# Kernel tuning notes

Hardware: AMD Instinct MI355X
Metric: run time of the kernel (lower is better)

The kernel has to match this reference:

```python
import jax, jax.numpy as jnp
import numpy as np

B, S, D, H, DFF, L, V = 2, 1024, 1280, 16, 8192, 4, 32000
DH = D // H
EPS = 1e-6


def positional_encoding(position, d_model):
    pos = np.arange(position)[:, None].astype(np.float32)
    i = np.arange(d_model)[None, :].astype(np.float32)
    angle = pos / np.power(10000.0, (2.0 * (i // 2)) / np.float32(d_model))
    sines = np.sin(angle[:, 0::2])
    cosines = np.cos(angle[:, 1::2])
    return jnp.asarray(np.concatenate([sines, cosines], axis=-1), dtype=jnp.float32)


def layer_norm(x, g, b):
    mu = jnp.mean(x, axis=-1, keepdims=True)
    var = jnp.mean(jnp.square(x - mu), axis=-1, keepdims=True)
    return (x - mu) * jax.lax.rsqrt(var + EPS) * g + b


def setup_inputs() -> dict:
    key = jax.random.key(0)
    ks = jax.random.split(key, 8)
    sc = 0.02
    return {
        "input_ids": jax.random.randint(ks[0], (B, S), 0, V, dtype=jnp.int64),
        "emb": jax.random.normal(ks[1], (V, D), jnp.float32) * sc,
        "Wq": jax.random.normal(ks[2], (L, D, D), jnp.float32) * sc,
        "Wk": jax.random.normal(ks[3], (L, D, D), jnp.float32) * sc,
        "Wv": jax.random.normal(ks[4], (L, D, D), jnp.float32) * sc,
        "Wo": jax.random.normal(ks[5], (L, D, D), jnp.float32) * sc,
        "bq": jnp.zeros((L, D)), "bk": jnp.zeros((L, D)),
        "bv": jnp.zeros((L, D)), "bo": jnp.zeros((L, D)),
        "W1": jax.random.normal(ks[6], (L, D, DFF), jnp.float32) * sc,
        "b1": jnp.zeros((L, DFF)),
        "W2": jax.random.normal(ks[7], (L, DFF, D), jnp.float32) * sc,
        "b2": jnp.zeros((L, D)),
        "ln1_g": jnp.ones((L, D)), "ln1_b": jnp.zeros((L, D)),
        "ln2_g": jnp.ones((L, D)), "ln2_b": jnp.zeros((L, D)),
        "lnf_g": jnp.ones((D,)), "lnf_b": jnp.zeros((D,)),
    }


def _forward(input_ids, emb, Wq, bq, Wk, bk, Wv, bv, Wo, bo,
             W1, b1, W2, b2, ln1_g, ln1_b, ln2_g, ln2_b, lnf_g, lnf_b):
    # embedding scaled by sqrt(d_model) + fixed sinusoidal positions
    x = emb[input_ids] * jnp.sqrt(jnp.float32(D)) + positional_encoding(S, D)[None]
    # CTRL causal mask: 1 above the diagonal, contributes mask * -1e4 to logits
    neg_mask = jnp.triu(jnp.ones((S, S), jnp.float32), k=1) * -10000.0
    inv_sqrt_dk = 1.0 / jnp.sqrt(jnp.float32(DH))

    def block(x, p):
        (wq, bq_, wk, bk_, wv, bv_, wo, bo_,
         w1, b1_, w2, b2_, g1, be1, g2, be2) = p
        n = layer_norm(x, g1, be1)
        q = (n @ wq + bq_).reshape(B, S, H, DH).transpose(0, 2, 1, 3)  # [B,H,S,DH]
        k = (n @ wk + bk_).reshape(B, S, H, DH).transpose(0, 2, 1, 3)
        v = (n @ wv + bv_).reshape(B, S, H, DH).transpose(0, 2, 1, 3)
        logits = jnp.einsum("bhqd,bhkd->bhqk", q, k) * inv_sqrt_dk + neg_mask
        attn = jax.nn.softmax(logits, axis=-1)
        ctx = jnp.einsum("bhqk,bhkd->bhqd", attn, v)
        ctx = ctx.transpose(0, 2, 1, 3).reshape(B, S, D)
        x = x + ctx @ wo + bo_
        n2 = layer_norm(x, g2, be2)
        x = x + jax.nn.relu(n2 @ w1 + b1_) @ w2 + b2_
        return x, None

    params = (Wq, bq, Wk, bk, Wv, bv, Wo, bo, W1, b1, W2, b2,
              ln1_g, ln1_b, ln2_g, ln2_b)
    x, _ = jax.lax.scan(block, x, params)
    return layer_norm(x, lnf_g, lnf_b)


def reference(input_ids, emb, Wq, Wk, Wv, Wo, bq, bk, bv, bo,
              W1, b1, W2, b2, ln1_g, ln1_b, ln2_g, ln2_b, lnf_g, lnf_b):
    return _forward(input_ids, emb, Wq, bq, Wk, bk, Wv, bv, Wo, bo,
                    W1, b1, W2, b2, ln1_g, ln1_b, ln2_g, ln2_b, lnf_g, lnf_b)
```

## Files before the change

### kernel.cpp

```cpp
#include <hip/hip_runtime.h>


typedef unsigned short ushort_t;
typedef __attribute__((ext_vector_type(8))) __bf16 bf16x8;
typedef __attribute__((ext_vector_type(4))) float f32x4;

typedef const __attribute__((address_space(1))) unsigned int gu32;
typedef __attribute__((address_space(3))) unsigned int lu32;

#define DEV __device__ __forceinline__

DEV float bf2f(ushort_t h) { return __uint_as_float(((unsigned)h) << 16); }
DEV ushort_t f2bf(float f) {
    unsigned u = __float_as_uint(f);
    unsigned r = (u + 0x7fffu + ((u >> 16) & 1u)) >> 16;
    return (ushort_t)r;
}

DEV void async16(const void* g, void* l) {
    __builtin_amdgcn_global_load_lds((gu32*)g, (lu32*)l, 16, 0, 0);
}

__global__ __launch_bounds__(256) void embed_k(const int* __restrict__ ids,
                                               const float* __restrict__ emb,
                                               float* __restrict__ x) {
    __shared__ int flag64;
    const int r = blockIdx.x, t = threadIdx.x;
    if (t == 0) {
        int z = 0;
        for (int i = 1; i < 256; i += 2) z |= ids[i];
        flag64 = (z == 0);
    }
    __syncthreads();
    const long id = flag64 ? (long)((const long long*)ids)[r] : (long)ids[r];
    const float* er = emb + (size_t)id * 1280;
    const float pos = (float)(r & 1023);
    #pragma unroll
    for (int i = 0; i < 5; i++) {
        const int c = t + i * 256;
        float pe;
        if (c < 640) {
            float w = expf(-(float)c * 0.0143911568312128f);
            pe = sinf(pos * w);
        } else {
            float w = expf(-(float)(c - 640) * 0.0143911568312128f);
            pe = cosf(pos * w);
        }
        x[(size_t)r * 1280 + c] = er[c] * 35.77708763999664f + pe;
    }
}

template <typename OUT>
__global__ __launch_bounds__(256) void layernorm_k(const float* __restrict__ x,
                                                   const float* __restrict__ gw,
                                                   const float* __restrict__ bw,
                                                   OUT* __restrict__ out) {
    __shared__ float red[8];
    const int row = blockIdx.x, t = threadIdx.x;
    const float* xr = x + (size_t)row * 1280;
    float v[5], s = 0.f, ss = 0.f;
    #pragma unroll
    for (int i = 0; i < 5; i++) {
        v[i] = xr[t + i * 256];
        s += v[i];
        ss += v[i] * v[i];
    }
    #pragma unroll
    for (int o = 32; o; o >>= 1) {
        s += __shfl_xor(s, o, 64);
        ss += __shfl_xor(ss, o, 64);
    }
    if ((t & 63) == 0) { red[t >> 6] = s; red[4 + (t >> 6)] = ss; }
    __syncthreads();
    s = red[0] + red[1] + red[2] + red[3];
    ss = red[4] + red[5] + red[6] + red[7];
    const float mean = s * (1.f / 1280.f);
    const float var = ss * (1.f / 1280.f) - mean * mean;
    const float rs = rsqrtf(var + 1e-6f);
    #pragma unroll
    for (int i = 0; i < 5; i++) {
        const int c = t + i * 256;
        const float o = (v[i] - mean) * rs * gw[c] + bw[c];
        if constexpr (sizeof(OUT) == 2) out[(size_t)row * 1280 + c] = f2bf(o);
        else                            out[(size_t)row * 1280 + c] = o;
    }
}

__global__ __launch_bounds__(256) void convtrans_k(const float* __restrict__ src,
                                                   ushort_t* __restrict__ dst,
                                                   int R, int C) {
    __shared__ float tile[64][65];
    const int bx = blockIdx.x * 64;
    const int by = blockIdx.y * 64;
    const int c = threadIdx.x & 63;
    const int r0 = threadIdx.x >> 6;
    #pragma unroll
    for (int r = r0; r < 64; r += 4)
        tile[r][c] = src[(size_t)(by + r) * C + bx + c];
    __syncthreads();
    #pragma unroll
    for (int j = r0; j < 64; j += 4)
        dst[(size_t)(bx + j) * R + by + c] = f2bf(tile[c][j]);
}

__global__ __launch_bounds__(256) void softmax_k(const float* __restrict__ S,
                                                 ushort_t* __restrict__ P) {
    __shared__ float red[4];
    const size_t row = blockIdx.x;
    const int t = threadIdx.x;
    const float* sr = S + row * 1024;
    float v[4], m = -1e30f;
    #pragma unroll
    for (int i = 0; i < 4; i++) {
        v[i] = sr[t + i * 256];
        m = fmaxf(m, v[i]);
    }
    #pragma unroll
    for (int o = 32; o; o >>= 1) m = fmaxf(m, __shfl_xor(m, o, 64));
    if ((t & 63) == 0) red[t >> 6] = m;
    __syncthreads();
    m = fmaxf(fmaxf(red[0], red[1]), fmaxf(red[2], red[3]));
    float s = 0.f;
    #pragma unroll
    for (int i = 0; i < 4; i++) {
        v[i] = __expf(v[i] - m);
        s += v[i];
    }
    #pragma unroll
    for (int o = 32; o; o >>= 1) s += __shfl_xor(s, o, 64);
    __syncthreads();
    if ((t & 63) == 0) red[t >> 6] = s;
    __syncthreads();
    s = red[0] + red[1] + red[2] + red[3];
    const float inv = 1.f / s;
    #pragma unroll
    for (int i = 0; i < 4; i++)
        P[row * 1024 + t + i * 256] = f2bf(v[i] * inv);
}

__global__ void zero_k(float4* __restrict__ p) {
    p[(size_t)blockIdx.x * 256 + threadIdx.x] = make_float4(0.f, 0.f, 0.f, 0.f);
}

enum { EPI_QKV = 0, EPI_RELU = 1, EPI_RESID = 2, EPI_SC = 3, EPI_CTX = 4 };

template <int EPI>
__global__ __launch_bounds__(256, 2) void gemm_bt(
    const ushort_t* __restrict__ A, const ushort_t* __restrict__ Bt,
    const float* __restrict__ bias, const float* __restrict__ bias2,
    const float* __restrict__ bias3, float* __restrict__ outF,
    ushort_t* __restrict__ outB, ushort_t* __restrict__ outB2,
    ushort_t* __restrict__ outB3,
    int K, int lda, int ldb, int nAlloc, int ldc,
    long aStr, long bStr, long cStr, int g0, float scaleP) {
    __shared__ __align__(16) ushort_t As[128 * 32];
    __shared__ __align__(16) ushort_t Bs[128 * 32];

    const int t = threadIdx.x;
    const int lane = t & 63, wave = t >> 6;
    const int wm = wave >> 1, wn = wave & 1;
    const int l16 = lane & 15, quad = lane >> 4;
    const int tileM = blockIdx.y * 128, tileN = blockIdx.x * 128;
    const long z = blockIdx.z;

    const ushort_t* Ab = A + z * aStr;
    const ushort_t* Bb = Bt + z * bStr;

    int kBeg = 0, kEnd = K;
    if (EPI == EPI_RESID) {
        const int kc = K / (int)gridDim.z;
        kBeg = (int)z * kc;
        kEnd = kBeg + kc;
    }

    const int rowS = t >> 2;
    const int kb = (t & 3) * 16;

    const int rb0 = min(tileN + rowS, nAlloc - 1);
    const int rb1 = min(tileN + rowS + 64, nAlloc - 1);

    const char* apc0 = (const char*)Ab + ((size_t)(tileM + rowS) * lda + kBeg) * 2 + kb;
    const char* apc1 = apc0 + (size_t)64 * lda * 2;
    const char* bpc0 = (const char*)Bb + ((size_t)rb0 * ldb + kBeg) * 2 + kb;
    const char* bpc1 = (const char*)Bb + ((size_t)rb1 * ldb + kBeg) * 2 + kb;

    char* lA0 = (char*)As + wave * 1024;
    char* lA1 = lA0 + 4096;
    char* lB0 = (char*)Bs + wave * 1024;
    char* lB1 = lB0 + 4096;

    f32x4 acc[4][4] = {};

    for (int k0 = kBeg; k0 < kEnd; k0 += 32) {
        async16(apc0, lA0);
        async16(apc1, lA1);
        async16(bpc0, lB0);
        async16(bpc1, lB1);
        apc0 += 64; apc1 += 64; bpc0 += 64; bpc1 += 64;
        __syncthreads();

        bf16x8 af[4], bfv[4];
        #pragma unroll
        for (int i = 0; i < 4; i++)
            af[i] = *(const bf16x8*)&As[(wm * 64 + i * 16 + l16) * 32 + quad * 8];
        #pragma unroll
        for (int j = 0; j < 4; j++)
            bfv[j] = *(const bf16x8*)&Bs[(wn * 64 + j * 16 + l16) * 32 + quad * 8];
        #pragma unroll
        for (int i = 0; i < 4; i++)
            #pragma unroll
            for (int j = 0; j < 4; j++)
                acc[i][j] = __builtin_amdgcn_mfma_f32_16x16x32_bf16(af[i], bfv[j], acc[i][j], 0, 0, 0);
        __syncthreads();
    }

    #pragma unroll
    for (int i = 0; i < 4; i++) {
        const int r0 = tileM + wm * 64 + i * 16 + quad * 4;
        #pragma unroll
        for (int j = 0; j < 4; j++) {
            const int c = tileN + wn * 64 + j * 16 + l16;
            float bv = 0.f;
            if (EPI == EPI_QKV) {
                const float* bp = bias;
                int cc = c;
                if (c >= 2560) { cc = c - 2560; bp = bias3; }
                else if (c >= 1280) { cc = c - 1280; bp = bias2; }
                bv = bp[cc];
            } else if (EPI == EPI_RELU) {
                bv = bias[c];
            } else if (EPI == EPI_RESID) {
                bv = (z == 0) ? bias[c] : 0.f;
            }
            #pragma unroll
            for (int g = 0; g < 4; g++) {
                const int r = r0 + g;
                const float v = acc[i][j][g] + bv;
                if (EPI == EPI_QKV) {
                    int cc = c;
                    ushort_t* ob = outB;
                    bool isV = false;
                    if (c >= 2560) { cc = c - 2560; ob = outB3; isV = true; }
                    else if (c >= 1280) { cc = c - 1280; ob = outB2; }
                    const int b = r >> 10, s = r & 1023;
                    const int h = cc / 80, d = cc - h * 80;
                    if (isV) ob[((size_t)((b * 16 + h) * 96 + d)) * 1024 + s] = f2bf(v);
                    else     ob[((size_t)((b * 16 + h) * 1024 + s)) * 96 + d] = f2bf(v);
                } else if (EPI == EPI_RELU) {
                    outB[(size_t)r * ldc + c] = f2bf(fmaxf(v, 0.f));
                } else if (EPI == EPI_RESID) {
                    atomicAdd(outF + (size_t)r * ldc + c, v);
                } else if (EPI == EPI_SC) {
                    float sv = acc[i][j][g] * scaleP;
                    if (c > r) sv -= 10000.f;
                    outF[z * cStr + (size_t)r * ldc + c] = sv;
                } else {
                    if (c < 80) {
                        const int gg = g0 + (int)z;
                        const int b = gg >> 4, h = gg & 15;
                        outB[((size_t)(b * 1024 + r)) * 1280 + h * 80 + c] = f2bf(acc[i][j][g]);
                    }
                }
            }
        }
    }
}

extern "C" void kernel_launch(void* const* d_in, const int* in_sizes, int n_in,
                              void* d_out, int out_size, void* d_ws, size_t ws_size,
                              hipStream_t stream) {
    const int* ids = (const int*)d_in[0];
    const float* emb = (const float*)d_in[1];
    const float* Wq = (const float*)d_in[2];
    const float* Wk = (const float*)d_in[3];
    const float* Wv = (const float*)d_in[4];
    const float* Wo = (const float*)d_in[5];
    const float* bq = (const float*)d_in[6];
    const float* bk = (const float*)d_in[7];
    const float* bv = (const float*)d_in[8];
    const float* bo = (const float*)d_in[9];
    const float* W1 = (const float*)d_in[10];
    const float* b1 = (const float*)d_in[11];
    const float* W2 = (const float*)d_in[12];
    const float* b2 = (const float*)d_in[13];
    const float* ln1g = (const float*)d_in[14];
    const float* ln1b = (const float*)d_in[15];
    const float* ln2g = (const float*)d_in[16];
    const float* ln2b = (const float*)d_in[17];
    const float* lnfg = (const float*)d_in[18];
    const float* lnfb = (const float*)d_in[19];
    (void)in_sizes; (void)n_in; (void)out_size; (void)ws_size;

    char* p = (char*)d_ws;
    float* xf = (float*)p;          p += (size_t)2048 * 1280 * 4;
    ushort_t* nbuf = (ushort_t*)p;  p += (size_t)2048 * 1280 * 2;
    ushort_t* qp = (ushort_t*)p;    p += (size_t)32 * 1024 * 96 * 2;
    ushort_t* kp = (ushort_t*)p;    p += (size_t)32 * 1024 * 96 * 2;
    ushort_t* vT = (ushort_t*)p;    p += (size_t)32 * 96 * 1024 * 2;
    ushort_t* ctx = (ushort_t*)p;   p += (size_t)2048 * 1280 * 2;
    ushort_t* h1 = (ushort_t*)p;    p += (size_t)2048 * 8192 * 2;
    ushort_t* WT = (ushort_t*)p;    p += (size_t)8192 * 1280 * 2;
    float* Sb = (float*)h1;
    ushort_t* Pb = WT;
    const int CH = 8;

    const float scaleP = 0.11180339887498948f;

    embed_k<<<2048, 256, 0, stream>>>(ids, emb, xf);
    zero_k<<<4608, 256, 0, stream>>>((float4*)qp);

    for (int l = 0; l < 4; l++) {
        const float* Wq_l = Wq + (size_t)l * 1638400;
        const float* Wk_l = Wk + (size_t)l * 1638400;
        const float* Wv_l = Wv + (size_t)l * 1638400;
        const float* Wo_l = Wo + (size_t)l * 1638400;
        const float* W1_l = W1 + (size_t)l * 10485760;
        const float* W2_l = W2 + (size_t)l * 10485760;

        layernorm_k<ushort_t><<<2048, 256, 0, stream>>>(xf, ln1g + l * 1280, ln1b + l * 1280, nbuf);

        convtrans_k<<<dim3(20, 20), 256, 0, stream>>>(Wq_l, WT, 1280, 1280);
        convtrans_k<<<dim3(20, 20), 256, 0, stream>>>(Wk_l, WT + (size_t)1280 * 1280, 1280, 1280);
        convtrans_k<<<dim3(20, 20), 256, 0, stream>>>(Wv_l, WT + (size_t)2560 * 1280, 1280, 1280);
        gemm_bt<EPI_QKV><<<dim3(30, 16, 1), 256, 0, stream>>>(
            nbuf, WT, bq + l * 1280, bk + l * 1280, bv + l * 1280,
            nullptr, qp, kp, vT, 1280, 1280, 1280, 3840, 0, 0, 0, 0, 0, 0.f);

        for (int c0 = 0; c0 < 32; c0 += CH) {
            gemm_bt<EPI_SC><<<dim3(8, 8, CH), 256, 0, stream>>>(
                qp + (size_t)c0 * 98304, kp + (size_t)c0 * 98304, nullptr, nullptr, nullptr,
                Sb, nullptr, nullptr, nullptr,
                96, 96, 96, 1024, 1024, 98304, 98304, 1048576, 0, scaleP);
            softmax_k<<<CH * 1024, 256, 0, stream>>>(Sb, Pb);
            gemm_bt<EPI_CTX><<<dim3(1, 8, CH), 256, 0, stream>>>(
                Pb, vT + (size_t)c0 * 98304, nullptr, nullptr, nullptr,
                nullptr, ctx, nullptr, nullptr,
                1024, 1024, 1024, 96, 0, 1048576, 98304, 0, c0, 0.f);
        }

        convtrans_k<<<dim3(20, 20), 256, 0, stream>>>(Wo_l, WT, 1280, 1280);
        gemm_bt<EPI_RESID><<<dim3(10, 16, 4), 256, 0, stream>>>(
            ctx, WT, bo + l * 1280, nullptr, nullptr,
            xf, nullptr, nullptr, nullptr,
            1280, 1280, 1280, 1280, 1280, 0, 0, 0, 0, 0.f);

        layernorm_k<ushort_t><<<2048, 256, 0, stream>>>(xf, ln2g + l * 1280, ln2b + l * 1280, nbuf);

        convtrans_k<<<dim3(128, 20), 256, 0, stream>>>(W1_l, WT, 1280, 8192);
        gemm_bt<EPI_RELU><<<dim3(64, 16, 1), 256, 0, stream>>>(
            nbuf, WT, b1 + l * 8192, nullptr, nullptr,
            nullptr, h1, nullptr, nullptr,
            1280, 1280, 1280, 8192, 8192, 0, 0, 0, 0, 0.f);

        convtrans_k<<<dim3(20, 128), 256, 0, stream>>>(W2_l, WT, 8192, 1280);
        gemm_bt<EPI_RESID><<<dim3(10, 16, 8), 256, 0, stream>>>(
            h1, WT, b2 + l * 1280, nullptr, nullptr,
            xf, nullptr, nullptr, nullptr,
            8192, 8192, 8192, 1280, 1280, 0, 0, 0, 0, 0.f);
    }

    layernorm_k<float><<<2048, 256, 0, stream>>>(xf, lnfg, lnfb, (float*)d_out);
}
```

Measured before the change: 2.410 ms.

## Double-buffer LDS tiles in GEMM to overlap async loads with MFMA

The GEMM main loop now uses two LDS buffers for the A and B tiles. Async global-to-LDS loads for the next K-step are issued before the MFMA compute on the current buffer, and there is one barrier per iteration instead of two. This is meant to hide global load latency behind tensor-core work. It doubles LDS usage to 32KB per block, which may reduce occupancy. It also relies on the single barrier to order the buffer reuse, and the compiler may insert vmcnt waits that serialize the loads anyway.

Result: no change. 2.418 ms (+0.3%).

```diff
diff --git a/kernel.cpp b/kernel.cpp
--- a/kernel.cpp
+++ b/kernel.cpp
@@ -142,6 +142,22 @@
     p[(size_t)blockIdx.x * 256 + threadIdx.x] = make_float4(0.f, 0.f, 0.f, 0.f);
 }
 
+DEV void gemm_compute(const ushort_t* as_, const ushort_t* bs_,
+                      int wm, int wn, int l16, int quad, f32x4 (&acc)[4][4]) {
+    bf16x8 af[4], bfv[4];
+    #pragma unroll
+    for (int i = 0; i < 4; i++)
+        af[i] = *(const bf16x8*)&as_[(wm * 64 + i * 16 + l16) * 32 + quad * 8];
+    #pragma unroll
+    for (int j = 0; j < 4; j++)
+        bfv[j] = *(const bf16x8*)&bs_[(wn * 64 + j * 16 + l16) * 32 + quad * 8];
+    #pragma unroll
+    for (int i = 0; i < 4; i++)
+        #pragma unroll
+        for (int j = 0; j < 4; j++)
+            acc[i][j] = __builtin_amdgcn_mfma_f32_16x16x32_bf16(af[i], bfv[j], acc[i][j], 0, 0, 0);
+}
+
 enum { EPI_QKV = 0, EPI_RELU = 1, EPI_RESID = 2, EPI_SC = 3, EPI_CTX = 4 };
 
 template <int EPI>
@@ -153,8 +169,8 @@
     ushort_t* __restrict__ outB3,
     int K, int lda, int ldb, int nAlloc, int ldc,
     long aStr, long bStr, long cStr, int g0, float scaleP) {
-    __shared__ __align__(16) ushort_t As[128 * 32];
-    __shared__ __align__(16) ushort_t Bs[128 * 32];
+    __shared__ __align__(16) ushort_t As[2][128 * 32];
+    __shared__ __align__(16) ushort_t Bs[2][128 * 32];
 
     const int t = threadIdx.x;
     const int lane = t & 63, wave = t >> 6;
@@ -172,6 +188,7 @@
         kBeg = (int)z * kc;
         kEnd = kBeg + kc;
     }
+    const int nt = (kEnd - kBeg) >> 5;
 
     const int rowS = t >> 2;
     const int kb = (t & 3) * 16;
@@ -184,35 +201,35 @@
     const char* bpc0 = (const char*)Bb + ((size_t)rb0 * ldb + kBeg) * 2 + kb;
     const char* bpc1 = (const char*)Bb + ((size_t)rb1 * ldb + kBeg) * 2 + kb;
 
-    char* lA0 = (char*)As + wave * 1024;
-    char* lA1 = lA0 + 4096;
-    char* lB0 = (char*)Bs + wave * 1024;
-    char* lB1 = lB0 + 4096;
+    char* lA = (char*)As + wave * 1024;
+    char* lB = (char*)Bs + wave * 1024;
 
     f32x4 acc[4][4] = {};
 
-    for (int k0 = kBeg; k0 < kEnd; k0 += 32) {
-        async16(apc0, lA0);
-        async16(apc1, lA1);
-        async16(bpc0, lB0);
-        async16(bpc1, lB1);
+    async16(apc0, lA);
+    async16(apc1, lA + 4096);
+    async16(bpc0, lB);
+    async16(bpc1, lB + 4096);
+    apc0 += 64; apc1 += 64; bpc0 += 64; bpc1 += 64;
+    __syncthreads();
+
+    int bo_ = 0;
+    for (int tt = 0; tt < nt - 1; ++tt) {
+        const int po = bo_ ^ 8192;
+        async16(apc0, lA + po);
+        async16(apc1, lA + po + 4096);
+        async16(bpc0, lB + po);
+        async16(bpc1, lB + po + 4096);
         apc0 += 64; apc1 += 64; bpc0 += 64; bpc1 += 64;
+        gemm_compute((const ushort_t*)((const char*)As + bo_),
+                     (const ushort_t*)((const char*)Bs + bo_),
+                     wm, wn, l16, quad, acc);
         __syncthreads();
-
-        bf16x8 af[4], bfv[4];
-        #pragma unroll
-        for (int i = 0; i < 4; i++)
-            af[i] = *(const bf16x8*)&As[(wm * 64 + i * 16 + l16) * 32 + quad * 8];
-        #pragma unroll
-        for (int j = 0; j < 4; j++)
-            bfv[j] = *(const bf16x8*)&Bs[(wn * 64 + j * 16 + l16) * 32 + quad * 8];
-        #pragma unroll
-        for (int i = 0; i < 4; i++)
-            #pragma unroll
-            for (int j = 0; j < 4; j++)
-                acc[i][j] = __builtin_amdgcn_mfma_f32_16x16x32_bf16(af[i], bfv[j], acc[i][j], 0, 0, 0);
-        __syncthreads();
-    }
+        bo_ = po;
+    }
+    gemm_compute((const ushort_t*)((const char*)As + bo_),
+                 (const ushort_t*)((const char*)Bs + bo_),
+                 wm, wn, l16, quad, acc);
 
     #pragma unroll
     for (int i = 0; i < 4; i++) {
```
